# Optimization experiments

Measured on AMD Instinct MI355X. Metric: run time of the kernel, lower is better.

## Reference

```python
import jax, jax.numpy as jnp
import numpy as np
import math

N_HEADS = 16
FACTOR = 5

def setup_inputs() -> dict:
    key = jax.random.key(0)
    ks = jax.random.split(key, 9)
    B, T, D = 4, 2048, 1024
    w = lambda k: jax.random.normal(k, (D, D), dtype=jnp.float32) * 0.02
    return {
        "x": jax.random.normal(ks[0], (B, T, D), dtype=jnp.float32),
        "Wq": w(ks[1]), "bq": jnp.zeros((D,), jnp.float32),
        "Wk": w(ks[2]), "bk": jnp.zeros((D,), jnp.float32),
        "Wv": w(ks[3]), "bv": jnp.zeros((D,), jnp.float32),
        "Wo": w(ks[4]), "bo": jnp.zeros((D,), jnp.float32),
    }

def reference(x, Wq, bq, Wk, bk, Wv, bv, Wo, bo):
    B, T, D = x.shape
    H = N_HEADS
    hd = D // H
    scale = hd ** (-0.5)

    def proj(W, b):
        # [B,T,D] -> [B,H,T,hd]
        return (x @ W + b).reshape(B, T, H, hd).transpose(0, 2, 1, 3)

    q = proj(Wq, bq)
    k = proj(Wk, bk)
    v = proj(Wv, bv)

    # top-u query selection by L1 norm per (b,h)
    u = min(int(FACTOR * math.log(T)), T)
    q_norm = jnp.sum(jnp.abs(q), axis=-1)          # [B,H,T]
    _, idx = jax.lax.top_k(q_norm, u)              # [B,H,u]

    # gather selected queries; compute only the u selected score rows
    q_sel = jnp.take_along_axis(q, idx[..., None], axis=2)  # [B,H,u,hd]
    sel_scores = jnp.einsum('bhud,bhtd->bhut', q_sel, k) * scale  # [B,H,u,T]

    # causal mask for selected rows: key pos j attends iff j <= query pos
    causal = jnp.arange(T)[None, None, None, :] <= idx[..., None]  # [B,H,u,T]
    sel_scores = jnp.where(causal, sel_scores, -jnp.inf)

    attn = jax.nn.softmax(sel_scores, axis=-1)     # dropout omitted (eval)
    sel_out = jnp.einsum('bhut,bhtd->bhud', attn, v)  # [B,H,u,hd]

    # scatter selected rows back into zeros (non-selected rows stay 0)
    bi = jnp.arange(B)[:, None, None]
    hi = jnp.arange(H)[None, :, None]
    attn_out = jnp.zeros((B, H, T, hd), x.dtype).at[bi, hi, idx].set(sel_out)

    out = attn_out.transpose(0, 2, 1, 3).reshape(B, T, D)
    return out @ Wo + bo
```

## Files before the change

### kernel.cpp

```cpp
#include <hip/hip_runtime.h>
#include <hip/hip_bf16.h>
#include <math.h>

#define B_  4
#define T_  2048
#define D_  1024
#define H_  16
#define HD_ 64
#define U_  38
#define M_  (B_*T_)
#define NCB_ 8
#define NC_ 64

typedef __attribute__((ext_vector_type(8))) short bf16x8;
typedef __attribute__((ext_vector_type(4))) float f32x4;

__device__ __forceinline__ short f2b(float f) {
    __hip_bfloat16 b = __float2bfloat16(f);
    return *(short*)&b;
}
__device__ __forceinline__ float b2f(short s) {
    __hip_bfloat16 b = *(__hip_bfloat16*)&s;
    return __bfloat162float(b);
}
__device__ __forceinline__ unsigned pack2(float lo, float hi) {
    unsigned a = (unsigned short)f2b(lo);
    unsigned b = ((unsigned)(unsigned short)f2b(hi)) << 16;
    return a | b;
}

__device__ __forceinline__ void gload16(const void* g, void* l) {
    __builtin_amdgcn_global_load_lds(
        (const __attribute__((address_space(1))) unsigned int*)g,
        (__attribute__((address_space(3))) unsigned int*)l,
        16, 0, 0);
}

__global__ __launch_bounds__(256) void conv_fused(
    const float* __restrict__ x,
    const float* __restrict__ Wq, const float* __restrict__ Wk,
    const float* __restrict__ Wv, const float* __restrict__ Wo,
    const float* __restrict__ bo,
    short* __restrict__ xh,
    short* __restrict__ wq2, short* __restrict__ wkvt, short* __restrict__ wot,
    float* __restrict__ out)
{
    __shared__ float tile[32][33];
    const int bid = blockIdx.x;
    if (bid < 8192) {
        const size_t i = ((size_t)bid * 256 + threadIdx.x) * 4;
        float4 v = *(const float4*)(x + i);
        short4 h;
        h.x = f2b(v.x); h.y = f2b(v.y); h.z = f2b(v.z); h.w = f2b(v.w);
        *(short4*)(xh + i) = h;
        return;
    }
    if (bid >= 12288) {
        const size_t i = (size_t)(bid - 12288) * 256 + threadIdx.x;
        float4 bv = *(const float4*)(bo + ((i & 255) << 2));
        *(float4*)(out + i * 4) = bv;
        return;
    }
    const int q = bid - 8192;
    const int which = q >> 10;
    const int by = (q & 1023) >> 5, bx = q & 31;
    const float* W = which == 0 ? Wq : (which == 1 ? Wk : (which == 2 ? Wv : Wo));
    const int k0 = by * 32, n0 = bx * 32;
    const int tx = threadIdx.x & 31, ty = threadIdx.x >> 5;
    #pragma unroll
    for (int r = ty; r < 32; r += 8)
        tile[r][tx] = W[(size_t)(k0 + r) * D_ + n0 + tx];
    __syncthreads();
    const int rr = threadIdx.x >> 3;
    const int kg = (threadIdx.x & 7) * 4;
    const float v0 = tile[kg + 0][rr], v1 = tile[kg + 1][rr];
    const float v2 = tile[kg + 2][rr], v3 = tile[kg + 3][rr];
    const size_t o = (size_t)(n0 + rr) * D_ + k0 + kg;
    if (which == 0) {
        short4 hi, lo;
        hi.x = f2b(v0); lo.x = f2b(v0 - b2f(hi.x));
        hi.y = f2b(v1); lo.y = f2b(v1 - b2f(hi.y));
        hi.z = f2b(v2); lo.z = f2b(v2 - b2f(hi.z));
        hi.w = f2b(v3); lo.w = f2b(v3 - b2f(hi.w));
        *(short4*)(wq2 + o) = hi;
        *(short4*)(wq2 + o + 1048576) = lo;
    } else {
        short4 p;
        p.x = f2b(v0); p.y = f2b(v1); p.z = f2b(v2); p.w = f2b(v3);
        if (which == 3) *(short4*)(wot + o) = p;
        else            *(short4*)(wkvt + (size_t)(which - 1) * D_ * D_ + o) = p;
    }
}

__global__ __launch_bounds__(256) void gemm_fused(
    const short* __restrict__ xh, const short* __restrict__ wq2,
    const short* __restrict__ wkvt,
    const float* __restrict__ bq, const float* __restrict__ bk,
    const float* __restrict__ bv,
    float* __restrict__ qnorm, short* __restrict__ kb, short* __restrict__ vt)
{
    __shared__ short As[128 * 128];
    __shared__ short Bs[128 * 128];
    const int bid = blockIdx.x;
    const bool isQ = bid < 512;
    const int tid = threadIdx.x, wid = tid >> 6, lane = tid & 63;
    const int l15 = lane & 15, gr = lane >> 4;
    const int lb = isQ ? bid : bid - 512;
    const int m0 = (lb & 63) * 128;
    const int n0 = (lb >> 6) * 128;
    const bool isK = !isQ && (n0 < D_);
    const int wr = (wid >> 1) * 64, wc = (wid & 1) * 64;

    f32x4 acc[4][4];
    #pragma unroll
    for (int i = 0; i < 4; ++i)
        #pragma unroll
        for (int j = 0; j < 4; ++j)
            acc[i][j] = (f32x4){0.f, 0.f, 0.f, 0.f};

    const short* Asrc = xh;
    const short* Bsrc = isQ ? wq2 : wkvt;

    for (int kt = 0; kt < 8; ++kt) {
        const int ka = kt * 128;
        #pragma unroll
        for (int i = 0; i < 8; ++i) {
            const int e = tid + i * 256;
            const int row = e >> 4;
            const int soff = ((e & 15) ^ (row & 15)) * 8;
            gload16(Asrc + (size_t)(m0 + row) * D_ + ka + soff,
                    (char*)As + i * 4096 + wid * 1024);
            gload16(Bsrc + (size_t)(n0 + row) * D_ + ka + soff,
                    (char*)Bs + i * 4096 + wid * 1024);
        }
        __syncthreads();
        #pragma unroll
        for (int ks = 0; ks < 4; ++ks) {
            bf16x8 a[4], b[4];
            #pragma unroll
            for (int i = 0; i < 4; ++i)
                a[i] = *(bf16x8*)((char*)As + (wr + i * 16 + l15) * 256
                                   + ((((ks << 2) | gr) ^ l15) * 16));
            #pragma unroll
            for (int j = 0; j < 4; ++j)
                b[j] = *(bf16x8*)((char*)Bs + (wc + j * 16 + l15) * 256
                                   + ((((ks << 2) | gr) ^ l15) * 16));
            if (isK) {
                #pragma unroll
                for (int i = 0; i < 4; ++i)
                    #pragma unroll
                    for (int j = 0; j < 4; ++j)
                        acc[i][j] = __builtin_amdgcn_mfma_f32_16x16x32_bf16(b[j], a[i], acc[i][j], 0, 0, 0);
            } else {
                #pragma unroll
                for (int i = 0; i < 4; ++i)
                    #pragma unroll
                    for (int j = 0; j < 4; ++j)
                        acc[i][j] = __builtin_amdgcn_mfma_f32_16x16x32_bf16(a[i], b[j], acc[i][j], 0, 0, 0);
            }
        }
        __syncthreads();
    }

    if (isQ) {
        const int h = (n0 + wc) >> 6;
        #pragma unroll
        for (int i = 0; i < 4; ++i)
            #pragma unroll
            for (int r = 0; r < 4; ++r) {
                int row = m0 + wr + i * 16 + gr * 4 + r;
                float s = 0.f;
                #pragma unroll
                for (int j = 0; j < 4; ++j) {
                    int col = n0 + wc + j * 16 + l15;
                    s += fabsf(acc[i][j][r] + bq[col]);
                }
                s += __shfl_xor(s, 1);
                s += __shfl_xor(s, 2);
                s += __shfl_xor(s, 4);
                s += __shfl_xor(s, 8);
                if (l15 == 0) {
                    int b = row >> 11, t = row & (T_ - 1);
                    qnorm[((size_t)b * H_ + h) * T_ + t] = s;
                }
            }
    } else if (isK) {
        #pragma unroll
        for (int i = 0; i < 4; ++i)
            #pragma unroll
            for (int j = 0; j < 4; ++j) {
                const int m = m0 + wr + i * 16 + l15;
                const int bb = m >> 11, t = m & (T_ - 1);
                const int n = n0 + wc + j * 16 + gr * 4;
                const int hh = n >> 6, dd = n & 63;
                float4 bias = *(const float4*)(bk + n);
                short4 pk;
                pk.x = f2b(acc[i][j][0] + bias.x);
                pk.y = f2b(acc[i][j][1] + bias.y);
                pk.z = f2b(acc[i][j][2] + bias.z);
                pk.w = f2b(acc[i][j][3] + bias.w);
                *(short4*)(kb + (((size_t)bb * H_ + hh) * T_ + t) * HD_ + dd) = pk;
            }
    } else {
        #pragma unroll
        for (int i = 0; i < 4; ++i)
            #pragma unroll
            for (int j = 0; j < 4; ++j) {
                const int col = n0 + wc + j * 16 + l15;
                const int rowb = m0 + wr + i * 16 + gr * 4;
                const int bb = rowb >> 11, t0 = rowb & (T_ - 1);
                const int cc2 = col - D_;
                const int hh = cc2 >> 6, dd = cc2 & 63;
                const float bias = bv[cc2];
                short4 pk;
                pk.x = f2b(acc[i][j][0] + bias);
                pk.y = f2b(acc[i][j][1] + bias);
                pk.z = f2b(acc[i][j][2] + bias);
                pk.w = f2b(acc[i][j][3] + bias);
                *(short4*)(vt + (((size_t)bb * H_ + hh) * HD_ + dd) * T_ + t0) = pk;
            }
    }
}

__global__ __launch_bounds__(64) void cand_kernel(
    const float* __restrict__ qnorm, int* __restrict__ cand)
{
    const int g = blockIdx.x;
    const int lane = threadIdx.x;
    unsigned v[32];
    const float* src = qnorm + (size_t)g * T_ + lane * 32;
    #pragma unroll
    for (int i = 0; i < 32; i += 4) {
        float4 t = *(const float4*)(src + i);
        v[i] = __float_as_uint(t.x); v[i + 1] = __float_as_uint(t.y);
        v[i + 2] = __float_as_uint(t.z); v[i + 3] = __float_as_uint(t.w);
    }
    unsigned lo = 0, hi = 0x7F800000u;
    while (lo < hi) {
        unsigned mid = lo + ((hi - lo) >> 1);
        int c = 0;
        #pragma unroll
        for (int i = 0; i < 32; ++i) c += (v[i] >= mid) ? 1 : 0;
        #pragma unroll
        for (int off = 1; off < 64; off <<= 1) c += __shfl_xor(c, off);
        if (c <= NC_) hi = mid; else lo = mid + 1;
    }
    const unsigned tau = lo;
    int myc = 0;
    #pragma unroll
    for (int i = 0; i < 32; ++i) myc += (v[i] >= tau) ? 1 : 0;
    int inc = myc;
    for (int off = 1; off < 64; off <<= 1) {
        int n = __shfl_up(inc, off);
        if (lane >= off) inc += n;
    }
    const int total = __shfl(inc, 63);
    int pos = inc - myc;
    #pragma unroll
    for (int i = 0; i < 32; ++i)
        if (v[i] >= tau) cand[g * NC_ + pos++] = lane * 32 + i;
    for (int p = total + lane; p < NC_; p += 64)
        cand[g * NC_ + p] = -1;
}

__global__ __launch_bounds__(64) void recheck_kernel(
    const float* __restrict__ x,
    const short* __restrict__ wq2, const float* __restrict__ bq,
    const int* __restrict__ cand,
    float* __restrict__ cnorm, short* __restrict__ candq)
{
    const int blk = blockIdx.x;
    const int g = blk >> 2, rt = blk & 3;
    const int b = g >> 4, h = g & 15;
    const int lane = threadIdx.x, l15 = lane & 15, gr = lane >> 4;

    const int aslot = rt * 16 + l15;
    int at = cand[g * NC_ + aslot];
    const float* xrow = x + ((size_t)b * T_ + (at < 0 ? 0 : at)) * D_;

    f32x4 acc[4];
    #pragma unroll
    for (int j = 0; j < 4; ++j) acc[j] = (f32x4){0.f, 0.f, 0.f, 0.f};

    const short* wqh = wq2;
    const short* wql = wq2 + 1048576;
    for (int kt = 0; kt < 32; ++kt) {
        const int k0 = kt * 32 + gr * 8;
        float4 xa = *(const float4*)(xrow + k0);
        float4 xb = *(const float4*)(xrow + k0 + 4);
        float xs[8] = {xa.x, xa.y, xa.z, xa.w, xb.x, xb.y, xb.z, xb.w};
        bf16x8 ah, al;
        #pragma unroll
        for (int e = 0; e < 8; ++e) {
            short hh = f2b(xs[e]);
            ah[e] = hh;
            al[e] = f2b(xs[e] - b2f(hh));
        }
        #pragma unroll
        for (int j = 0; j < 4; ++j) {
            const size_t wrow = (size_t)(h * HD_ + j * 16 + l15) * D_ + k0;
            bf16x8 bh = *(const bf16x8*)(wqh + wrow);
            bf16x8 bl = *(const bf16x8*)(wql + wrow);
            acc[j] = __builtin_amdgcn_mfma_f32_16x16x32_bf16(ah, bh, acc[j], 0, 0, 0);
            acc[j] = __builtin_amdgcn_mfma_f32_16x16x32_bf16(ah, bl, acc[j], 0, 0, 0);
            acc[j] = __builtin_amdgcn_mfma_f32_16x16x32_bf16(al, bh, acc[j], 0, 0, 0);
        }
    }

    #pragma unroll
    for (int r = 0; r < 4; ++r) {
        const int slot = rt * 16 + gr * 4 + r;
        float s = 0.f;
        #pragma unroll
        for (int j = 0; j < 4; ++j) {
            const int col = j * 16 + l15;
            float val = acc[j][r] + bq[h * HD_ + col];
            candq[((size_t)g * NC_ + slot) * HD_ + col] = f2b(val);
            s += fabsf(val);
        }
        s += __shfl_xor(s, 1);
        s += __shfl_xor(s, 2);
        s += __shfl_xor(s, 4);
        s += __shfl_xor(s, 8);
        if (l15 == 0) {
            int ct = cand[g * NC_ + slot];
            cnorm[g * NC_ + slot] = (ct < 0) ? -3e38f : s;
        }
    }
}

__global__ __launch_bounds__(64) void topk38_kernel(
    const float* __restrict__ cnorm, const int* __restrict__ cand,
    int* __restrict__ idxb, int* __restrict__ slotb)
{
    const int g = blockIdx.x;
    const int lane = threadIdx.x;
    float v = cnorm[g * NC_ + lane];
    int c = cand[g * NC_ + lane];
    int tt = (c < 0) ? (1 << 30) : c;
    if (c < 0) v = -3e38f;
    bool fl = false;
    for (int it = 0; it < U_; ++it) {
        float bv = v; int bt = tt; int bs = lane;
        for (int off = 32; off; off >>= 1) {
            float ov = __shfl_xor(bv, off);
            int ot = __shfl_xor(bt, off);
            int os = __shfl_xor(bs, off);
            if (ov > bv || (ov == bv && ot < bt)) { bv = ov; bt = ot; bs = os; }
        }
        if (bs == lane) { v = -3e38f; fl = true; }
    }
    unsigned long long bm = __ballot(fl);
    unsigned long long lowmask = ((unsigned long long)1 << lane) - 1;
    if (fl) {
        int p = __popcll(bm & lowmask);
        idxb[g * U_ + p] = tt;
        slotb[g * 40 + p] = lane;
    }
}

__global__ __launch_bounds__(256) void attn_part(
    const short* __restrict__ candq, const int* __restrict__ slotb,
    const short* __restrict__ kb, const short* __restrict__ vt,
    const int* __restrict__ idxb,
    float* __restrict__ pm, float* __restrict__ pl, float* __restrict__ po)
{
    __shared__ short qs[48 * 72];
    __shared__ __align__(16) char shbuf[40448];
    __shared__ int sidx[48];
    short* pls  = (short*)shbuf;
    float* redo = (float*)shbuf;
    float* redm = (float*)(shbuf + 38912);
    float* redl = (float*)(shbuf + 39680);

    const int bid = blockIdx.x;
    const int g = bid & 63;
    const int c = bid >> 6;
    const int tid = threadIdx.x, wid = tid >> 6, lane = tid & 63;
    const int l15 = lane & 15, gr = lane >> 4;
    const int j0w = (c * 4 + wid) * 64;

    if (tid < 48) sidx[tid] = (tid < U_) ? idxb[g * U_ + tid] : 0;
    __syncthreads();
    for (int e = tid; e < 48 * 16; e += 256) {
        int u = e >> 4, d4 = e & 15;
        short4 v = make_short4(0, 0, 0, 0);
        if (u < U_) {
            int slot = slotb[g * 40 + u];
            v = *(const short4*)(candq + ((size_t)g * NC_ + slot) * HD_ + d4 * 4);
        }
        *(short4*)&qs[u * 72 + d4 * 4] = v;
    }
    __syncthreads();

    bool skp[3];
    #pragma unroll
    for (int uf = 0; uf < 3; ++uf) {
        int mi = uf * 16 + 15; if (mi >= U_) mi = U_ - 1;
        skp[uf] = (sidx[mi] < j0w);
    }

    int su[3];
    #pragma unroll
    for (int uf = 0; uf < 3; ++uf) su[uf] = sidx[uf * 16 + l15];

    f32x4 accs[3][4];
    #pragma unroll
    for (int uf = 0; uf < 3; ++uf)
        #pragma unroll
        for (int jf = 0; jf < 4; ++jf)
            accs[uf][jf] = (f32x4){0.f, 0.f, 0.f, 0.f};

    bf16x8 ka[4][2];
    #pragma unroll
    for (int jf = 0; jf < 4; ++jf)
        #pragma unroll
        for (int ks = 0; ks < 2; ++ks)
            ka[jf][ks] = *(const bf16x8*)(kb + ((size_t)g * T_ + j0w + jf * 16 + l15) * HD_ + ks * 32 + gr * 8);

    #pragma unroll
    for (int uf = 0; uf < 3; ++uf) {
        if (!skp[uf]) {
            bf16x8 q0 = *(bf16x8*)&qs[(uf * 16 + l15) * 72 + gr * 8];
            bf16x8 q1 = *(bf16x8*)&qs[(uf * 16 + l15) * 72 + 32 + gr * 8];
            #pragma unroll
            for (int jf = 0; jf < 4; ++jf) {
                accs[uf][jf] = __builtin_amdgcn_mfma_f32_16x16x32_bf16(ka[jf][0], q0, accs[uf][jf], 0, 0, 0);
                accs[uf][jf] = __builtin_amdgcn_mfma_f32_16x16x32_bf16(ka[jf][1], q1, accs[uf][jf], 0, 0, 0);
            }
        }
    }

    short* pw = pls + wid * 48 * 72;
    #pragma unroll
    for (int uf = 0; uf < 3; ++uf) {
        if (skp[uf]) {
            if (gr == 0) {
                int u = uf * 16 + l15;
                redm[wid * 48 + u] = -1e30f;
                redl[wid * 48 + u] = 0.f;
            }
        } else {
            float mm = -3e38f;
            #pragma unroll
            for (int jf = 0; jf < 4; ++jf)
                #pragma unroll
                for (int r = 0; r < 4; ++r) {
                    int j = j0w + jf * 16 + gr * 4 + r;
                    float s = accs[uf][jf][r] * 0.125f;
                    s = (j <= su[uf]) ? s : -1e30f;
                    accs[uf][jf][r] = s;
                    mm = fmaxf(mm, s);
                }
            mm = fmaxf(mm, __shfl_xor(mm, 16));
            mm = fmaxf(mm, __shfl_xor(mm, 32));
            float ll = 0.f;
            #pragma unroll
            for (int jf = 0; jf < 4; ++jf)
                #pragma unroll
                for (int r = 0; r < 4; ++r) {
                    float e = __expf(accs[uf][jf][r] - mm);
                    accs[uf][jf][r] = e;
                    ll += e;
                }
            ll += __shfl_xor(ll, 16);
            ll += __shfl_xor(ll, 32);
            if (gr == 0) {
                int u = uf * 16 + l15;
                redm[wid * 48 + u] = mm;
                redl[wid * 48 + u] = ll;
            }
            #pragma unroll
            for (int jf = 0; jf < 4; ++jf) {
                uint2 wv;
                wv.x = pack2(accs[uf][jf][0], accs[uf][jf][1]);
                wv.y = pack2(accs[uf][jf][2], accs[uf][jf][3]);
                *(uint2*)&pw[(uf * 16 + l15) * 72 + jf * 16 + gr * 4] = wv;
            }
        }
    }

    bf16x8 va[4][2];
    #pragma unroll
    for (int df = 0; df < 4; ++df)
        #pragma unroll
        for (int ks = 0; ks < 2; ++ks)
            va[df][ks] = *(const bf16x8*)(vt + ((size_t)g * HD_ + df * 16 + l15) * T_ + j0w + ks * 32 + gr * 8);

    f32x4 acco[4][3];
    #pragma unroll
    for (int df = 0; df < 4; ++df)
        #pragma unroll
        for (int uf = 0; uf < 3; ++uf)
            acco[df][uf] = (f32x4){0.f, 0.f, 0.f, 0.f};
    #pragma unroll
    for (int uf = 0; uf < 3; ++uf) {
        if (!skp[uf]) {
            bf16x8 p0 = *(bf16x8*)&pw[(uf * 16 + l15) * 72 + gr * 8];
            bf16x8 p1 = *(bf16x8*)&pw[(uf * 16 + l15) * 72 + 32 + gr * 8];
            #pragma unroll
            for (int df = 0; df < 4; ++df) {
                acco[df][uf] = __builtin_amdgcn_mfma_f32_16x16x32_bf16(va[df][0], p0, acco[df][uf], 0, 0, 0);
                acco[df][uf] = __builtin_amdgcn_mfma_f32_16x16x32_bf16(va[df][1], p1, acco[df][uf], 0, 0, 0);
            }
        }
    }

    __syncthreads();

    #pragma unroll
    for (int df = 0; df < 4; ++df)
        #pragma unroll
        for (int uf = 0; uf < 3; ++uf) {
            int u = uf * 16 + l15;
            if (u < U_) {
                float4 o;
                o.x = acco[df][uf][0]; o.y = acco[df][uf][1];
                o.z = acco[df][uf][2]; o.w = acco[df][uf][3];
                *(float4*)&redo[((size_t)(wid * 38 + u)) * 64 + df * 16 + gr * 4] = o;
            }
        }
    __syncthreads();

    for (int e = tid; e < U_ * 64; e += 256) {
        int u = e >> 6, d = e & 63;
        float m0 = redm[u], m1 = redm[48 + u], m2 = redm[96 + u], m3 = redm[144 + u];
        float m = fmaxf(fmaxf(m0, m1), fmaxf(m2, m3));
        float e0 = __expf(m0 - m), e1 = __expf(m1 - m), e2 = __expf(m2 - m), e3 = __expf(m3 - m);
        float l = redl[u] * e0 + redl[48 + u] * e1 + redl[96 + u] * e2 + redl[144 + u] * e3;
        float o = redo[(size_t)u * 64 + d] * e0
                + redo[(size_t)(38 + u) * 64 + d] * e1
                + redo[(size_t)(76 + u) * 64 + d] * e2
                + redo[(size_t)(114 + u) * 64 + d] * e3;
        po[((size_t)(g * NCB_ + c) * U_ + u) * HD_ + d] = o;
        if (d == 0) {
            pm[(size_t)(g * NCB_ + c) * U_ + u] = m;
            pl[(size_t)(g * NCB_ + c) * U_ + u] = l;
        }
    }
}

__global__ __launch_bounds__(256) void oproj_kernel(
    const float* __restrict__ pm, const float* __restrict__ pl,
    const float* __restrict__ po, const int* __restrict__ idxb,
    const short* __restrict__ wot, float* __restrict__ out)
{
    __shared__ short sel[48 * 72];
    __shared__ int st[48];
    __shared__ float swl[U_][NCB_];
    const int g = blockIdx.x;
    const int ny = blockIdx.y;
    const int b = g >> 4, h = g & 15;
    const int tid = threadIdx.x, w = tid >> 6, lane = tid & 63;
    const int l15 = lane & 15, gr = lane >> 4;

    if (tid < 48) st[tid] = (tid < U_) ? idxb[g * U_ + tid] : 0;
    if (tid < U_) {
        float mc[NCB_], lc[NCB_];
        #pragma unroll
        for (int c = 0; c < NCB_; ++c) {
            mc[c] = pm[(size_t)(g * NCB_ + c) * U_ + tid];
            lc[c] = pl[(size_t)(g * NCB_ + c) * U_ + tid];
        }
        float m = -3e38f;
        #pragma unroll
        for (int c = 0; c < NCB_; ++c) m = fmaxf(m, mc[c]);
        float wv[NCB_], l = 0.f;
        #pragma unroll
        for (int c = 0; c < NCB_; ++c) { wv[c] = __expf(mc[c] - m); l += lc[c] * wv[c]; }
        float inv = 1.f / l;
        #pragma unroll
        for (int c = 0; c < NCB_; ++c) swl[tid][c] = wv[c] * inv;
    }
    for (int e = tid; e < 48 * 16; e += 256) {
        int u = e >> 4, d4 = e & 15;
        if (u >= U_) *(short4*)&sel[u * 72 + d4 * 4] = make_short4(0, 0, 0, 0);
    }
    __syncthreads();

    for (int e = tid; e < U_ * 64; e += 256) {
        int u = e >> 6, d = e & 63;
        float o = 0.f;
        #pragma unroll
        for (int c = 0; c < NCB_; ++c)
            o += po[((size_t)(g * NCB_ + c) * U_ + u) * HD_ + d] * swl[u][c];
        sel[u * 72 + d] = f2b(o);
    }
    __syncthreads();

    bf16x8 a[3][2];
    #pragma unroll
    for (int uf = 0; uf < 3; ++uf)
        #pragma unroll
        for (int ks = 0; ks < 2; ++ks)
            a[uf][ks] = *(bf16x8*)&sel[(uf * 16 + l15) * 72 + ks * 32 + gr * 8];

    for (int nf = 0; nf < 8; ++nf) {
        const int n0 = ny * 512 + w * 128 + nf * 16;
        bf16x8 bf[2];
        #pragma unroll
        for (int ks = 0; ks < 2; ++ks)
            bf[ks] = *(const bf16x8*)(wot + (size_t)(n0 + l15) * D_ + h * HD_ + ks * 32 + gr * 8);
        f32x4 acc[3];
        #pragma unroll
        for (int uf = 0; uf < 3; ++uf) {
            acc[uf] = (f32x4){0.f, 0.f, 0.f, 0.f};
            acc[uf] = __builtin_amdgcn_mfma_f32_16x16x32_bf16(a[uf][0], bf[0], acc[uf], 0, 0, 0);
            acc[uf] = __builtin_amdgcn_mfma_f32_16x16x32_bf16(a[uf][1], bf[1], acc[uf], 0, 0, 0);
        }
        #pragma unroll
        for (int uf = 0; uf < 3; ++uf)
            #pragma unroll
            for (int r = 0; r < 4; ++r) {
                int u = uf * 16 + gr * 4 + r;
                if (u < U_)
                    atomicAdd(out + ((size_t)b * T_ + st[u]) * D_ + n0 + l15, acc[uf][r]);
            }
    }
}

extern "C" void kernel_launch(void* const* d_in, const int* in_sizes, int n_in,
                              void* d_out, int out_size, void* d_ws, size_t ws_size,
                              hipStream_t stream)
{
    const float* x  = (const float*)d_in[0];
    const float* Wq = (const float*)d_in[1];
    const float* bq = (const float*)d_in[2];
    const float* Wk = (const float*)d_in[3];
    const float* bk = (const float*)d_in[4];
    const float* Wv = (const float*)d_in[5];
    const float* bv = (const float*)d_in[6];
    const float* Wo = (const float*)d_in[7];
    const float* bo = (const float*)d_in[8];
    float* out = (float*)d_out;

    char* ws = (char*)d_ws;
    short* xh    = (short*)(ws);
    short* wq2   = (short*)(ws + 33554432);
    short* wkvt  = (short*)(ws + 37748736);
    short* kb    = (short*)(ws + 41943040);
    short* vt    = (short*)(ws + 58720256);
    float* qnorm = (float*)(ws + 75497472);
    int*   idxb  = (int*)  (ws + 76021760);
    int*   cand  = (int*)  (ws + 76660736);
    float* cnorm = (float*)(ws + 76697600);
    int*   slotb = (int*)  (ws + 76734464);
    short* candq = (short*)(ws + 76750848);
    short* wot   = (short*)(ws + 77930496);
    float* po    = (float*)(ws);
    float* pm    = (float*)(ws + 19922944);
    float* pl    = (float*)(ws + 20234240);

    conv_fused<<<8192 + 4096 + 8192, 256, 0, stream>>>(x, Wq, Wk, Wv, Wo, bo,
                                                       xh, wq2, wkvt, wot, out);
    gemm_fused<<<1536, 256, 0, stream>>>(xh, wq2, wkvt, bq, bk, bv, qnorm, kb, vt);
    cand_kernel<<<B_ * H_, 64, 0, stream>>>(qnorm, cand);
    recheck_kernel<<<B_ * H_ * 4, 64, 0, stream>>>(x, wq2, bq, cand, cnorm, candq);
    topk38_kernel<<<B_ * H_, 64, 0, stream>>>(cnorm, cand, idxb, slotb);
    attn_part<<<64 * NCB_, 256, 0, stream>>>(candq, slotb, kb, vt, idxb, pm, pl, po);
    oproj_kernel<<<dim3(B_ * H_, 2), 256, 0, stream>>>(pm, pl, po, idxb, wot, out);
}
```

Before: 173.2 us.

## Fold top-38 selection into attention and oproj kernels; split recheck K across two waves

Removes the standalone topk38 kernel launch and the idxb/slotb buffers. The wave-level top-38 selection is now recomputed redundantly in the first wave of every attn_part and oproj block. recheck_kernel now uses two waves per block, each covering half of the K range, and combines the partial accumulators through LDS. This saves one launch and shortens the serial recheck loop, at the cost of repeated top-k shuffle work in each consuming block and an extra LDS reduction.

```diff
diff --git a/kernel.cpp b/kernel.cpp
--- a/kernel.cpp
+++ b/kernel.cpp
@@ -34,6 +34,35 @@
         (const __attribute__((address_space(1))) unsigned int*)g,
         (__attribute__((address_space(3))) unsigned int*)l,
         16, 0, 0);
+}
+
+__device__ __forceinline__ void wave_topk38(
+    const float* __restrict__ cnorm, const int* __restrict__ cand,
+    int g, int lane, int* sidx_lds, int* slot_lds)
+{
+    if (lane < 48) { sidx_lds[lane] = 0; if (slot_lds) slot_lds[lane] = 0; }
+    float v = cnorm[g * NC_ + lane];
+    int c = cand[g * NC_ + lane];
+    int tt = (c < 0) ? (1 << 30) : c;
+    if (c < 0) v = -3e38f;
+    bool fl = false;
+    for (int it = 0; it < U_; ++it) {
+        float bv = v; int bt = tt; int bs = lane;
+        for (int off = 32; off; off >>= 1) {
+            float ov = __shfl_xor(bv, off);
+            int ot = __shfl_xor(bt, off);
+            int os = __shfl_xor(bs, off);
+            if (ov > bv || (ov == bv && ot < bt)) { bv = ov; bt = ot; bs = os; }
+        }
+        if (bs == lane) { v = -3e38f; fl = true; }
+    }
+    unsigned long long bm = __ballot(fl);
+    unsigned long long lowmask = ((unsigned long long)1 << lane) - 1;
+    if (fl) {
+        int p = __popcll(bm & lowmask);
+        sidx_lds[p] = tt;
+        if (slot_lds) slot_lds[p] = lane;
+    }
 }
 
 __global__ __launch_bounds__(256) void conv_fused(
@@ -263,16 +292,18 @@
         cand[g * NC_ + p] = -1;
 }
 
-__global__ __launch_bounds__(64) void recheck_kernel(
+__global__ __launch_bounds__(128) void recheck_kernel(
     const float* __restrict__ x,
     const short* __restrict__ wq2, const float* __restrict__ bq,
     const int* __restrict__ cand,
     float* __restrict__ cnorm, short* __restrict__ candq)
 {
+    __shared__ float lacc[128 * 20];
     const int blk = blockIdx.x;
     const int g = blk >> 2, rt = blk & 3;
     const int b = g >> 4, h = g & 15;
-    const int lane = threadIdx.x, l15 = lane & 15, gr = lane >> 4;
+    const int tid = threadIdx.x, w = tid >> 6, lane = tid & 63;
+    const int l15 = lane & 15, gr = lane >> 4;
 
     const int aslot = rt * 16 + l15;
     int at = cand[g * NC_ + aslot];
@@ -284,7 +315,7 @@
 
     const short* wqh = wq2;
     const short* wql = wq2 + 1048576;
-    for (int kt = 0; kt < 32; ++kt) {
+    for (int kt = w * 16; kt < w * 16 + 16; ++kt) {
         const int k0 = kt * 32 + gr * 8;
         float4 xa = *(const float4*)(xrow + k0);
         float4 xb = *(const float4*)(xrow + k0 + 4);
@@ -308,6 +339,19 @@
     }
 
     #pragma unroll
+    for (int j = 0; j < 4; ++j)
+        *(f32x4*)&lacc[tid * 20 + j * 4] = acc[j];
+    __syncthreads();
+    if (w != 0) return;
+
+    #pragma unroll
+    for (int j = 0; j < 4; ++j) {
+        f32x4 p0 = *(f32x4*)&lacc[lane * 20 + j * 4];
+        f32x4 p1 = *(f32x4*)&lacc[(lane + 64) * 20 + j * 4];
+        acc[j] = p0 + p1;
+    }
+
+    #pragma unroll
     for (int r = 0; r < 4; ++r) {
         const int slot = rt * 16 + gr * 4 + r;
         float s = 0.f;
@@ -329,45 +373,16 @@
     }
 }
 
-__global__ __launch_bounds__(64) void topk38_kernel(
+__global__ __launch_bounds__(256) void attn_part(
+    const short* __restrict__ candq,
     const float* __restrict__ cnorm, const int* __restrict__ cand,
-    int* __restrict__ idxb, int* __restrict__ slotb)
-{
-    const int g = blockIdx.x;
-    const int lane = threadIdx.x;
-    float v = cnorm[g * NC_ + lane];
-    int c = cand[g * NC_ + lane];
-    int tt = (c < 0) ? (1 << 30) : c;
-    if (c < 0) v = -3e38f;
-    bool fl = false;
-    for (int it = 0; it < U_; ++it) {
-        float bv = v; int bt = tt; int bs = lane;
-        for (int off = 32; off; off >>= 1) {
-            float ov = __shfl_xor(bv, off);
-            int ot = __shfl_xor(bt, off);
-            int os = __shfl_xor(bs, off);
-            if (ov > bv || (ov == bv && ot < bt)) { bv = ov; bt = ot; bs = os; }
-        }
-        if (bs == lane) { v = -3e38f; fl = true; }
-    }
-    unsigned long long bm = __ballot(fl);
-    unsigned long long lowmask = ((unsigned long long)1 << lane) - 1;
-    if (fl) {
-        int p = __popcll(bm & lowmask);
-        idxb[g * U_ + p] = tt;
-        slotb[g * 40 + p] = lane;
-    }
-}
-
-__global__ __launch_bounds__(256) void attn_part(
-    const short* __restrict__ candq, const int* __restrict__ slotb,
     const short* __restrict__ kb, const short* __restrict__ vt,
-    const int* __restrict__ idxb,
     float* __restrict__ pm, float* __restrict__ pl, float* __restrict__ po)
 {
     __shared__ short qs[48 * 72];
     __shared__ __align__(16) char shbuf[40448];
     __shared__ int sidx[48];
+    __shared__ int ssl[48];
     short* pls  = (short*)shbuf;
     float* redo = (float*)shbuf;
     float* redm = (float*)(shbuf + 38912);
@@ -380,13 +395,13 @@
     const int l15 = lane & 15, gr = lane >> 4;
     const int j0w = (c * 4 + wid) * 64;
 
-    if (tid < 48) sidx[tid] = (tid < U_) ? idxb[g * U_ + tid] : 0;
+    if (wid == 0) wave_topk38(cnorm, cand, g, lane, sidx, ssl);
     __syncthreads();
     for (int e = tid; e < 48 * 16; e += 256) {
         int u = e >> 4, d4 = e & 15;
         short4 v = make_short4(0, 0, 0, 0);
         if (u < U_) {
-            int slot = slotb[g * 40 + u];
+            int slot = ssl[u];
             v = *(const short4*)(candq + ((size_t)g * NC_ + slot) * HD_ + d4 * 4);
         }
         *(short4*)&qs[u * 72 + d4 * 4] = v;
@@ -542,7 +557,8 @@
 
 __global__ __launch_bounds__(256) void oproj_kernel(
     const float* __restrict__ pm, const float* __restrict__ pl,
-    const float* __restrict__ po, const int* __restrict__ idxb,
+    const float* __restrict__ po,
+    const float* __restrict__ cnorm, const int* __restrict__ cand,
     const short* __restrict__ wot, float* __restrict__ out)
 {
     __shared__ short sel[48 * 72];
@@ -554,7 +570,7 @@
     const int tid = threadIdx.x, w = tid >> 6, lane = tid & 63;
     const int l15 = lane & 15, gr = lane >> 4;
 
-    if (tid < 48) st[tid] = (tid < U_) ? idxb[g * U_ + tid] : 0;
+    if (w == 0) wave_topk38(cnorm, cand, g, lane, st, (int*)0);
     if (tid < U_) {
         float mc[NCB_], lc[NCB_];
         #pragma unroll
@@ -641,10 +657,8 @@
     short* kb    = (short*)(ws + 41943040);
     short* vt    = (short*)(ws + 58720256);
     float* qnorm = (float*)(ws + 75497472);
-    int*   idxb  = (int*)  (ws + 76021760);
     int*   cand  = (int*)  (ws + 76660736);
     float* cnorm = (float*)(ws + 76697600);
-    int*   slotb = (int*)  (ws + 76734464);
     short* candq = (short*)(ws + 76750848);
     short* wot   = (short*)(ws + 77930496);
     float* po    = (float*)(ws);
@@ -655,8 +669,7 @@
                                                        xh, wq2, wkvt, wot, out);
     gemm_fused<<<1536, 256, 0, stream>>>(xh, wq2, wkvt, bq, bk, bv, qnorm, kb, vt);
     cand_kernel<<<B_ * H_, 64, 0, stream>>>(qnorm, cand);
-    recheck_kernel<<<B_ * H_ * 4, 64, 0, stream>>>(x, wq2, bq, cand, cnorm, candq);
-    topk38_kernel<<<B_ * H_, 64, 0, stream>>>(cnorm, cand, idxb, slotb);
-    attn_part<<<64 * NCB_, 256, 0, stream>>>(candq, slotb, kb, vt, idxb, pm, pl, po);
-    oproj_kernel<<<dim3(B_ * H_, 2), 256, 0, stream>>>(pm, pl, po, idxb, wot, out);
-}
+    recheck_kernel<<<B_ * H_ * 4, 128, 0, stream>>>(x, wq2, bq, cand, cnorm, candq);
+    attn_part<<<64 * NCB_, 256, 0, stream>>>(candq, cnorm, cand, kb, vt, pm, pl, po);
+    oproj_kernel<<<dim3(B_ * H_, 2), 256, 0, stream>>>(pm, pl, po, cnorm, cand, wot, out);
+}
```

After: 190.7 us. 10.1% more time.
